# Optimization experiments

Hardware: AMD Instinct MI355X
Metric: run time of the kernel (lower is better)

Reference implementation:

```python
import jax, jax.numpy as jnp
import numpy as np

BATCH = 65536
VEC = 512       # CLIP embedding dim
K = 1024        # num_cluster
GAMMA = 0.99
EPS = 1e-05


def setup_inputs() -> dict:
    key = jax.random.key(0)
    k1, k2, k3 = jax.random.split(key, 3)
    batch_vectors = jax.random.normal(k1, (BATCH, VEC), dtype=jnp.float32)
    weight = jax.random.normal(k2, (VEC, K), dtype=jnp.float32)        # codebook, stored (vec_size, num_cluster)
    cluster_size = jnp.ones((K,), dtype=jnp.float32)
    embed_avg = jax.random.normal(k3, (VEC, K), dtype=jnp.float32)
    return {
        "batch_vectors": batch_vectors,
        "weight": weight,
        "cluster_size": cluster_size,
        "embed_avg": embed_avg,
    }


def reference(batch_vectors, weight, cluster_size, embed_avg):
    """One minibatch_update step of clusteringEMA_torch.

    Returns the updated codebook `weight` of shape (vec_size, num_cluster).
    """
    gamma = GAMMA
    eps = EPS
    num_cluster = weight.shape[1]

    # nearest centroid: squared L2 distance has the same argmin as the L2 norm
    x2 = jnp.sum(batch_vectors * batch_vectors, axis=1, keepdims=True)   # (B,1)
    w2 = jnp.sum(weight * weight, axis=0)[None, :]                       # (1,K)
    dist2 = x2 + w2 - 2.0 * (batch_vectors @ weight)                     # (B,K)
    argmin = jnp.argmin(dist2, axis=-1)                                  # (B,)

    # per-cluster counts (one-hot sum), zeros replaced by 1
    counts = jnp.zeros((num_cluster,), dtype=batch_vectors.dtype).at[argmin].add(1.0)
    n_idx_choice = jnp.where(counts == 0, 1.0, counts)

    # EMA of cluster sizes
    new_cluster_size = gamma * cluster_size + (1.0 - gamma) * n_idx_choice

    # embed_sum = x^T @ onehot  == per-cluster sum of assigned vectors, (vec,K)
    embed_sum = jax.ops.segment_sum(batch_vectors, argmin, num_segments=num_cluster).T
    new_embed_avg = gamma * embed_avg + (1.0 - gamma) * embed_sum

    # Laplace-smoothed normalization
    n = jnp.sum(new_cluster_size)
    cs = (new_cluster_size + eps) / (n + num_cluster * eps) * n
    new_weight = new_embed_avg / cs[None, :]
    return new_weight
```

## Files before the change

kernel.cpp:

```cpp
#include <hip/hip_runtime.h>

typedef unsigned int uint;
typedef unsigned short ushort_t;
typedef unsigned long long u64;
typedef __attribute__((ext_vector_type(4))) float f32x4;
typedef __attribute__((ext_vector_type(8))) __bf16 bf16x8;
typedef __attribute__((ext_vector_type(8))) unsigned short us8;

#define BATCH 65536
#define VEC 512
#define K 1024
#define GAMMA 0.99f
#define EPS 1e-05f
#define SEG 64

#define BM 256
#define BN 256
#define NKT (VEC / 32)
#define BSLOT 2048

__device__ __forceinline__ ushort_t hi_of(float f) {
    return (ushort_t)(__float_as_uint(f) >> 16);
}
__device__ __forceinline__ ushort_t lo_of(float f) {
    float fhi = __uint_as_float(__float_as_uint(f) & 0xffff0000u);
    return (ushort_t)(__float_as_uint(f - fhi) >> 16);
}

__device__ __forceinline__ void gl16(const void* g, void* l) {
    __builtin_amdgcn_global_load_lds(
        (const __attribute__((address_space(1))) unsigned int*)g,
        (__attribute__((address_space(3))) unsigned int*)l, 16, 0, 0);
}

__device__ __forceinline__ void cvt8(f32x4 q0, f32x4 q1, bf16x8& h, bf16x8& l) {
    float ff[8] = {q0[0], q0[1], q0[2], q0[3], q1[0], q1[1], q1[2], q1[3]};
    us8 hh, ll;
#pragma unroll
    for (int j = 0; j < 8; ++j) {
        hh[j] = hi_of(ff[j]);
        ll[j] = lo_of(ff[j]);
    }
    h = __builtin_bit_cast(bf16x8, hh);
    l = __builtin_bit_cast(bf16x8, ll);
}

__global__ void k_w2(const float* __restrict__ w, float* __restrict__ w2) {
    __shared__ float red[16][17];
    const int c = blockIdx.x * 16 + (threadIdx.x & 15);
    const int vg = threadIdx.x >> 4;
    float s = 0.f;
    for (int i = 0; i < 32; ++i) {
        float t = w[(size_t)(vg * 32 + i) * K + c];
        s += t * t;
    }
    red[vg][threadIdx.x & 15] = s;
    __syncthreads();
    if (vg == 0) {
        float acc = 0.f;
#pragma unroll
        for (int g = 0; g < 16; ++g) acc += red[g][threadIdx.x & 15];
        w2[c] = acc;
    }
}

__global__ void k_pack_w(const float* __restrict__ w, us8* __restrict__ wpk) {
    const int g = blockIdx.x;
    const int gx = g >> 4, ks = g & 15;
    const int t = threadIdx.x;
    us8* dst = wpk + (size_t)g * BSLOT;
#pragma unroll
    for (int i = 0; i < 8; ++i) {
        const int o = i * 256 + t;
        const int lane = o & 63, half = (o >> 6) & 1, ct = o >> 7;
        const int col = gx * BN + ct * 16 + (lane & 15);
        const int kb = ks * 32 + (lane >> 4) * 8;
        us8 v;
#pragma unroll
        for (int j = 0; j < 8; ++j) {
            float f = w[(size_t)(kb + j) * K + col];
            v[j] = half ? lo_of(f) : hi_of(f);
        }
        dst[o] = v;
    }
}

__launch_bounds__(512, 2)
__global__ void k_gemm256(const float* __restrict__ x, const us8* __restrict__ wpk,
                          const float* __restrict__ w2, u64* __restrict__ keys) {
    __shared__ us8 lds[2][4096];

    const int blk = blockIdx.x;
    const int gy = (blk & 7) * 32 + (blk >> 5);
    const int gx = (blk >> 3) & 3;
    const int t = threadIdx.x;
    const int lane = t & 63;
    const int wv = t >> 6;
    const int wm = wv >> 2;
    const int wn = wv & 3;

    const us8* bsrc = wpk + (size_t)gx * (NKT * BSLOT);

    auto stage = [&](int buf, int kt) {
#pragma unroll
        for (int i = 0; i < 4; ++i) {
            const int g16 = i * 512 + t;
            const int slab = g16 >> 7, kh = (g16 >> 6) & 1, l = g16 & 63;
            const int row = gy * BM + slab * 16 + (l & 15);
            const int k = kt * 32 + ((l >> 4) << 3) + (kh << 2);
            gl16(x + (size_t)row * VEC + k, &lds[buf][g16]);
        }
        const us8* sb = bsrc + (size_t)kt * BSLOT;
#pragma unroll
        for (int i = 0; i < 4; ++i)
            gl16(sb + i * 512 + t, &lds[buf][2048 + i * 512 + t]);
    };

    f32x4 acc[8][4];
#pragma unroll
    for (int i = 0; i < 8; ++i)
#pragma unroll
        for (int j = 0; j < 4; ++j) acc[i][j] = (f32x4){0.f, 0.f, 0.f, 0.f};

    stage(0, 0);
    __syncthreads();

    for (int tk = 0; tk < NKT; ++tk) {
        const int buf = tk & 1;
        if (tk + 1 < NKT) stage(buf ^ 1, tk + 1);

        const us8* A = &lds[buf][0];
        const us8* B = &lds[buf][2048];

        bf16x8 bh[4], bl[4];
#pragma unroll
        for (int ct = 0; ct < 4; ++ct) {
            const int o = (wn * 4 + ct) * 128 + lane;
            bh[ct] = __builtin_bit_cast(bf16x8, B[o]);
            bl[ct] = __builtin_bit_cast(bf16x8, B[o + 64]);
        }
#pragma unroll
        for (int p = 0; p < 4; ++p) {
            bf16x8 ah[2], al[2];
#pragma unroll
            for (int i = 0; i < 2; ++i) {
                const int slab = wm * 8 + p * 2 + i;
                f32x4 q0 = __builtin_bit_cast(f32x4, A[slab * 128 + lane]);
                f32x4 q1 = __builtin_bit_cast(f32x4, A[slab * 128 + 64 + lane]);
                cvt8(q0, q1, ah[i], al[i]);
            }
#pragma unroll
            for (int i = 0; i < 2; ++i)
#pragma unroll
                for (int ct = 0; ct < 4; ++ct) {
                    const int m = p * 2 + i;
                    acc[m][ct] = __builtin_amdgcn_mfma_f32_16x16x32_bf16(ah[i], bh[ct], acc[m][ct], 0, 0, 0);
                    acc[m][ct] = __builtin_amdgcn_mfma_f32_16x16x32_bf16(ah[i], bl[ct], acc[m][ct], 0, 0, 0);
                    acc[m][ct] = __builtin_amdgcn_mfma_f32_16x16x32_bf16(al[i], bh[ct], acc[m][ct], 0, 0, 0);
                }
        }
        __syncthreads();
    }

    const int col_base = gx * BN + wn * 64;
    float w2c[4];
#pragma unroll
    for (int ct = 0; ct < 4; ++ct) w2c[ct] = w2[col_base + ct * 16 + (lane & 15)];

#pragma unroll
    for (int rt = 0; rt < 8; ++rt) {
#pragma unroll
        for (int reg = 0; reg < 4; ++reg) {
            u64 km = ~0ull;
#pragma unroll
            for (int ct = 0; ct < 4; ++ct) {
                float dist = w2c[ct] - 2.0f * acc[rt][ct][reg];
                uint su = __float_as_uint(dist);
                su = (su & 0x80000000u) ? ~su : (su | 0x80000000u);
                const int col = col_base + ct * 16 + (lane & 15);
                u64 key = ((u64)su << 32) | (uint)col;
                km = key < km ? key : km;
            }
#pragma unroll
            for (int m = 1; m < 16; m <<= 1) {
                u64 o = __shfl_xor((unsigned long long)km, m);
                km = o < km ? o : km;
            }
            if ((lane & 15) == 0) {
                const int row = gy * BM + wm * 128 + rt * 16 + (lane >> 4) * 4 + reg;
                atomicMin((unsigned long long*)&keys[row], (unsigned long long)km);
            }
        }
    }
}

__global__ void k_hist(const u64* __restrict__ keys, int* __restrict__ counts) {
    const int b = blockIdx.x * blockDim.x + threadIdx.x;
    atomicAdd(&counts[(uint)(keys[b] & 0xffffffffull)], 1);
}

__global__ void k_scan(const int* __restrict__ counts,
                       const float* __restrict__ cluster_size,
                       int* __restrict__ offsets, float* __restrict__ cs) {
    __shared__ int wsum[16];
    __shared__ float fw[16];
    const int t = threadIdx.x;
    const int lane = t & 63, wid = t >> 6;
    const int c = counts[t];

    int s = c;
#pragma unroll
    for (int d = 1; d < 64; d <<= 1) {
        int o = __shfl_up(s, d);
        if (lane >= d) s += o;
    }
    float ncs = GAMMA * cluster_size[t] + (1.0f - GAMMA) * ((c == 0) ? 1.0f : (float)c);
    float fs = ncs;
#pragma unroll
    for (int d = 32; d > 0; d >>= 1) fs += __shfl_xor(fs, d);

    if (lane == 63) wsum[wid] = s;
    if (lane == 0) fw[wid] = fs;
    __syncthreads();
    if (wid == 0 && lane < 16) {
        int v = wsum[lane];
#pragma unroll
        for (int d = 1; d < 16; d <<= 1) {
            int o = __shfl_up(v, d);
            if (lane >= d) v += o;
        }
        wsum[lane] = v;
    }
    __syncthreads();
    const int base = wid ? wsum[wid - 1] : 0;
    offsets[t] = base + s - c;

    float n = 0.f;
#pragma unroll
    for (int i = 0; i < 16; ++i) n += fw[i];
    cs[t] = (ncs + EPS) / (n + (float)K * EPS) * n;
}

__global__ void k_scatter(const u64* __restrict__ keys, const int* __restrict__ offsets,
                          int* __restrict__ cursor, int* __restrict__ sorted,
                          int* __restrict__ sortedk) {
    const int b = blockIdx.x * blockDim.x + threadIdx.x;
    const int k = (int)(uint)(keys[b] & 0xffffffffull);
    const int pos = atomicAdd(&cursor[k], 1);
    sorted[offsets[k] + pos] = b;
    sortedk[offsets[k] + pos] = k;
}

__launch_bounds__(512)
__global__ void k_segred(const float* __restrict__ x, const int* __restrict__ sorted,
                         const int* __restrict__ sortedk, float* __restrict__ esum) {
    __shared__ int srow[SEG];
    __shared__ int skid[SEG];
    const int b = blockIdx.x;
    const int t = threadIdx.x;
    if (t < SEG) {
        srow[t] = sorted[b * SEG + t];
        skid[t] = sortedk[b * SEG + t];
    }
    __syncthreads();

    float a = 0.f;
    int cur = skid[0];
#pragma unroll 8
    for (int i = 0; i < SEG; ++i) {
        const int k = skid[i];
        if (k != cur) {
            atomicAdd(&esum[(size_t)cur * VEC + t], a);
            a = 0.f;
            cur = k;
        }
        a += x[(size_t)srow[i] * VEC + t];
    }
    atomicAdd(&esum[(size_t)cur * VEC + t], a);
}

__launch_bounds__(256)
__global__ void k_finalize(const float* __restrict__ esum, const float* __restrict__ embed_avg,
                           const float* __restrict__ cs, float* __restrict__ out) {
    __shared__ float tile[64][65];
    const int k0 = blockIdx.x * 64;
    const int v0 = blockIdx.y * 64;
    const int c = threadIdx.x & 63;
    const int r0 = threadIdx.x >> 6;
#pragma unroll
    for (int j = 0; j < 16; ++j) {
        const int r = r0 + j * 4;
        tile[r][c] = esum[(size_t)(k0 + r) * VEC + v0 + c];
    }
    __syncthreads();
    const float csk = cs[k0 + c];
#pragma unroll
    for (int j = 0; j < 16; ++j) {
        const int r = r0 + j * 4;
        const size_t o = (size_t)(v0 + r) * K + k0 + c;
        out[o] = (GAMMA * embed_avg[o] + (1.0f - GAMMA) * tile[c][r]) / csk;
    }
}

extern "C" void kernel_launch(void* const* d_in, const int* in_sizes, int n_in,
                              void* d_out, int out_size, void* d_ws, size_t ws_size,
                              hipStream_t stream) {
    const float* x            = (const float*)d_in[0];
    const float* w            = (const float*)d_in[1];
    const float* cluster_size = (const float*)d_in[2];
    const float* embed_avg    = (const float*)d_in[3];
    float* out = (float*)d_out;

    u64*   keys    = (u64*)d_ws;
    float* w2      = (float*)(keys + BATCH);
    float* cs      = w2 + K;
    int*   counts  = (int*)(cs + K);
    int*   cursor  = counts + K;
    int*   offsets = cursor + K;
    int*   sorted  = offsets + K;
    int*   sortedk = sorted + BATCH;
    float* esum    = (float*)(sortedk + BATCH);
    us8*   wpk     = (us8*)(esum + (size_t)K * VEC);

    hipMemsetAsync(keys, 0xFF, (size_t)BATCH * sizeof(u64), stream);
    hipMemsetAsync(counts, 0, 2 * K * sizeof(int), stream);
    hipMemsetAsync(esum, 0, (size_t)K * VEC * sizeof(float), stream);

    k_w2<<<K / 16, 256, 0, stream>>>(w, w2);
    k_pack_w<<<64, 256, 0, stream>>>(w, wpk);
    k_gemm256<<<(BATCH / BM) * (K / BN), 512, 0, stream>>>(x, wpk, w2, keys);
    k_hist<<<BATCH / 256, 256, 0, stream>>>(keys, counts);
    k_scan<<<1, K, 0, stream>>>(counts, cluster_size, offsets, cs);
    k_scatter<<<BATCH / 256, 256, 0, stream>>>(keys, offsets, cursor, sorted, sortedk);
    k_segred<<<BATCH / SEG, 512, 0, stream>>>(x, sorted, sortedk, esum);
    k_finalize<<<dim3(K / 64, VEC / 64), 256, 0, stream>>>(esum, embed_avg, cs, out);
}
```

Before: 462.6 us.

## Fuse weight-norm and memsets into pack kernel; pre-convert A tiles once into LDS

Merges the w2 norm computation into the weight-packing kernel, which now stages W through shared memory and writes 16 partial sums that the GEMM epilogue adds up. The three memsets are removed: pack_w initialises keys and counts, and the histogram kernel zeroes esum. In the GEMM, x tiles are loaded through registers and split into bf16 hi/lo once before being written to LDS, so each wave no longer repeats the conversion on every LDS read. This trades async global-to-LDS loads for register-staged loads and adds a 16-way w2 reduction per column in the epilogue.

After: 455.8 us. Within noise of the previous version (-1.5%).

```diff
diff --git a/kernel.cpp b/kernel.cpp
--- a/kernel.cpp
+++ b/kernel.cpp
@@ -45,50 +45,50 @@
     l = __builtin_bit_cast(bf16x8, ll);
 }
 
-__global__ void k_w2(const float* __restrict__ w, float* __restrict__ w2) {
-    __shared__ float red[16][17];
-    const int c = blockIdx.x * 16 + (threadIdx.x & 15);
-    const int vg = threadIdx.x >> 4;
-    float s = 0.f;
-    for (int i = 0; i < 32; ++i) {
-        float t = w[(size_t)(vg * 32 + i) * K + c];
-        s += t * t;
-    }
-    red[vg][threadIdx.x & 15] = s;
-    __syncthreads();
-    if (vg == 0) {
-        float acc = 0.f;
-#pragma unroll
-        for (int g = 0; g < 16; ++g) acc += red[g][threadIdx.x & 15];
-        w2[c] = acc;
-    }
-}
-
-__global__ void k_pack_w(const float* __restrict__ w, us8* __restrict__ wpk) {
+__global__ void k_pack_w(const float* __restrict__ w, us8* __restrict__ wpk,
+                         float* __restrict__ w2p, u64* __restrict__ keys,
+                         int* __restrict__ cc ) {
+    __shared__ float lds[32][257];
     const int g = blockIdx.x;
     const int gx = g >> 4, ks = g & 15;
     const int t = threadIdx.x;
-    us8* dst = wpk + (size_t)g * BSLOT;
+
+#pragma unroll
+    for (int r = 0; r < 32; ++r)
+        lds[r][t] = w[(size_t)(ks * 32 + r) * K + gx * 256 + t];
+    __syncthreads();
+
+    float s = 0.f;
+#pragma unroll
+    for (int r = 0; r < 32; ++r) { float f = lds[r][t]; s += f * f; }
+    w2p[ks * K + gx * 256 + t] = s;
+
 #pragma unroll
     for (int i = 0; i < 8; ++i) {
         const int o = i * 256 + t;
         const int lane = o & 63, half = (o >> 6) & 1, ct = o >> 7;
-        const int col = gx * BN + ct * 16 + (lane & 15);
-        const int kb = ks * 32 + (lane >> 4) * 8;
+        const int cl = ct * 16 + (lane & 15);
+        const int r0 = (lane >> 4) * 8;
         us8 v;
 #pragma unroll
         for (int j = 0; j < 8; ++j) {
-            float f = w[(size_t)(kb + j) * K + col];
+            float f = lds[r0 + j][cl];
             v[j] = half ? lo_of(f) : hi_of(f);
         }
-        dst[o] = v;
-    }
+        wpk[(size_t)g * BSLOT + o] = v;
+    }
+
+    u64* kp = keys + (size_t)g * 1024;
+#pragma unroll
+    for (int i = 0; i < 4; ++i) kp[i * 256 + t] = ~0ull;
+    if (g < 8) cc[g * 256 + t] = 0;
 }
 
 __launch_bounds__(512, 2)
 __global__ void k_gemm256(const float* __restrict__ x, const us8* __restrict__ wpk,
-                          const float* __restrict__ w2, u64* __restrict__ keys) {
-    __shared__ us8 lds[2][4096];
+                          const float* __restrict__ w2p, u64* __restrict__ keys) {
+    __shared__ us8 a_lds[2][2048];
+    __shared__ us8 b_lds[2][2048];
 
     const int blk = blockIdx.x;
     const int gy = (blk & 7) * 32 + (blk >> 5);
@@ -101,19 +101,35 @@
 
     const us8* bsrc = wpk + (size_t)gx * (NKT * BSLOT);
 
-    auto stage = [&](int buf, int kt) {
-#pragma unroll
-        for (int i = 0; i < 4; ++i) {
-            const int g16 = i * 512 + t;
-            const int slab = g16 >> 7, kh = (g16 >> 6) & 1, l = g16 & 63;
-            const int row = gy * BM + slab * 16 + (l & 15);
-            const int k = kt * 32 + ((l >> 4) << 3) + (kh << 2);
-            gl16(x + (size_t)row * VEC + k, &lds[buf][g16]);
-        }
+    const int slab0 = t >> 6;
+    const int ls = t & 63;
+    const float* xrow0 = x + (size_t)(gy * BM + slab0 * 16 + (ls & 15)) * VEC + (ls >> 4) * 8;
+    const float* xrow1 = xrow0 + (size_t)128 * VEC;
+
+    f32x4 av[4];
+    auto aload = [&](int kt) {
+        const float* p0 = xrow0 + kt * 32;
+        av[0] = *(const f32x4*)(p0);
+        av[1] = *(const f32x4*)(p0 + 4);
+        const float* p1 = xrow1 + kt * 32;
+        av[2] = *(const f32x4*)(p1);
+        av[3] = *(const f32x4*)(p1 + 4);
+    };
+    auto awrite = [&](int buf) {
+        bf16x8 h0, l0, h1, l1;
+        cvt8(av[0], av[1], h0, l0);
+        cvt8(av[2], av[3], h1, l1);
+        const int o = slab0 * 128 + ls;
+        a_lds[buf][o]          = __builtin_bit_cast(us8, h0);
+        a_lds[buf][o + 64]     = __builtin_bit_cast(us8, l0);
+        a_lds[buf][o + 1024]       = __builtin_bit_cast(us8, h1);
+        a_lds[buf][o + 1024 + 64]  = __builtin_bit_cast(us8, l1);
+    };
+    auto bstage = [&](int buf, int kt) {
         const us8* sb = bsrc + (size_t)kt * BSLOT;
 #pragma unroll
         for (int i = 0; i < 4; ++i)
-            gl16(sb + i * 512 + t, &lds[buf][2048 + i * 512 + t]);
+            gl16(sb + i * 512 + t, &b_lds[buf][i * 512 + t]);
     };
 
     f32x4 acc[8][4];
@@ -122,15 +138,21 @@
 #pragma unroll
         for (int j = 0; j < 4; ++j) acc[i][j] = (f32x4){0.f, 0.f, 0.f, 0.f};
 
-    stage(0, 0);
+    aload(0);
+    bstage(0, 0);
+    awrite(0);
     __syncthreads();
 
     for (int tk = 0; tk < NKT; ++tk) {
         const int buf = tk & 1;
-        if (tk + 1 < NKT) stage(buf ^ 1, tk + 1);
-
-        const us8* A = &lds[buf][0];
-        const us8* B = &lds[buf][2048];
+        const bool nx = (tk + 1 < NKT);
+        if (nx) {
+            aload(tk + 1);
+            bstage(buf ^ 1, tk + 1);
+        }
+
+        const us8* A = &a_lds[buf][0];
+        const us8* B = &b_lds[buf][0];
 
         bf16x8 bh[4], bl[4];
 #pragma unroll
@@ -144,10 +166,9 @@
             bf16x8 ah[2], al[2];
 #pragma unroll
             for (int i = 0; i < 2; ++i) {
-                const int slab = wm * 8 + p * 2 + i;
-                f32x4 q0 = __builtin_bit_cast(f32x4, A[slab * 128 + lane]);
-                f32x4 q1 = __builtin_bit_cast(f32x4, A[slab * 128 + 64 + lane]);
-                cvt8(q0, q1, ah[i], al[i]);
+                const int o = (wm * 8 + p * 2 + i) * 128 + lane;
+                ah[i] = __builtin_bit_cast(bf16x8, A[o]);
+                al[i] = __builtin_bit_cast(bf16x8, A[o + 64]);
             }
 #pragma unroll
             for (int i = 0; i < 2; ++i)
@@ -159,13 +180,20 @@
                     acc[m][ct] = __builtin_amdgcn_mfma_f32_16x16x32_bf16(al[i], bh[ct], acc[m][ct], 0, 0, 0);
                 }
         }
+        if (nx) awrite(buf ^ 1);
         __syncthreads();
     }
 
     const int col_base = gx * BN + wn * 64;
     float w2c[4];
 #pragma unroll
-    for (int ct = 0; ct < 4; ++ct) w2c[ct] = w2[col_base + ct * 16 + (lane & 15)];
+    for (int ct = 0; ct < 4; ++ct) {
+        const int col = col_base + ct * 16 + (lane & 15);
+        float s = 0.f;
+#pragma unroll
+        for (int p = 0; p < 16; ++p) s += w2p[p * K + col];
+        w2c[ct] = s;
+    }
 
 #pragma unroll
     for (int rt = 0; rt < 8; ++rt) {
@@ -194,8 +222,12 @@
     }
 }
 
-__global__ void k_hist(const u64* __restrict__ keys, int* __restrict__ counts) {
+__global__ void k_hist(const u64* __restrict__ keys, int* __restrict__ counts,
+                       float* __restrict__ esum) {
     const int b = blockIdx.x * blockDim.x + threadIdx.x;
+    f32x4 z = {0.f, 0.f, 0.f, 0.f};
+    ((f32x4*)esum)[b * 2]     = z;
+    ((f32x4*)esum)[b * 2 + 1] = z;
     atomicAdd(&counts[(uint)(keys[b] & 0xffffffffull)], 1);
 }
 
@@ -312,8 +344,8 @@
     float* out = (float*)d_out;
 
     u64*   keys    = (u64*)d_ws;
-    float* w2      = (float*)(keys + BATCH);
-    float* cs      = w2 + K;
+    float* w2p     = (float*)(keys + BATCH);
+    float* cs      = w2p + 16 * K;
     int*   counts  = (int*)(cs + K);
     int*   cursor  = counts + K;
     int*   offsets = cursor + K;
@@ -322,14 +354,9 @@
     float* esum    = (float*)(sortedk + BATCH);
     us8*   wpk     = (us8*)(esum + (size_t)K * VEC);
 
-    hipMemsetAsync(keys, 0xFF, (size_t)BATCH * sizeof(u64), stream);
-    hipMemsetAsync(counts, 0, 2 * K * sizeof(int), stream);
-    hipMemsetAsync(esum, 0, (size_t)K * VEC * sizeof(float), stream);
-
-    k_w2<<<K / 16, 256, 0, stream>>>(w, w2);
-    k_pack_w<<<64, 256, 0, stream>>>(w, wpk);
-    k_gemm256<<<(BATCH / BM) * (K / BN), 512, 0, stream>>>(x, wpk, w2, keys);
-    k_hist<<<BATCH / 256, 256, 0, stream>>>(keys, counts);
+    k_pack_w<<<64, 256, 0, stream>>>(w, wpk, w2p, keys, counts);
+    k_gemm256<<<(BATCH / BM) * (K / BN), 512, 0, stream>>>(x, wpk, w2p, keys);
+    k_hist<<<BATCH / 256, 256, 0, stream>>>(keys, counts, esum);
     k_scan<<<1, K, 0, stream>>>(counts, cluster_size, offsets, cs);
     k_scatter<<<BATCH / 256, 256, 0, stream>>>(keys, offsets, cursor, sorted, sortedk);
     k_segred<<<BATCH / SEG, 512, 0, stream>>>(x, sorted, sortedk, esum);
```
